# Kernel tuning notes

Hardware: AMD Instinct MI355X
Metric: run time of the kernel (lower is better)

## Reference

```python
import jax, jax.numpy as jnp
import numpy as np

SEQ = 8192
IN_DIM = 1024
HIDDEN_DIM = 2048
N_EXPERTS = 8
TOPK = 2


def setup_inputs() -> dict:
    key = jax.random.key(0)
    ks = jax.random.split(key, 6)
    scale = 0.02
    inp = jax.random.normal(ks[0], (SEQ, IN_DIM), jnp.float32)
    weights = jax.random.uniform(ks[1], (SEQ, TOPK), jnp.float32)
    selections = jax.random.randint(ks[2], (SEQ, TOPK), 0, N_EXPERTS, jnp.int32)
    up_proj = jax.random.normal(ks[3], (HIDDEN_DIM * N_EXPERTS, IN_DIM), jnp.float32) * scale
    gate_proj = jax.random.normal(ks[4], (HIDDEN_DIM * N_EXPERTS, IN_DIM), jnp.float32) * scale
    down_proj = jax.random.normal(ks[5], (HIDDEN_DIM * N_EXPERTS, IN_DIM), jnp.float32) * scale
    return {"inp": inp, "weights": weights, "up_proj": up_proj,
            "gate_proj": gate_proj, "down_proj": down_proj, "selections": selections}


def reference(inp, weights, up_proj, gate_proj, down_proj, selections):
    seq, in_dim = inp.shape
    topk = selections.shape[-1]
    # dispatch: replicate each token topk times -> (seq*topk, in_dim)
    x = jnp.broadcast_to(inp[:, None, :], (seq, topk, in_dim)).reshape(-1, in_dim)
    e_ids = selections.reshape(-1)  # (seq*topk,) expert id per dispatched token
    W_up = up_proj.reshape(N_EXPERTS, HIDDEN_DIM, in_dim)
    W_gate = gate_proj.reshape(N_EXPERTS, HIDDEN_DIM, in_dim)
    W_down = down_proj.reshape(N_EXPERTS, HIDDEN_DIM, in_dim)
    out = jnp.zeros_like(x)
    # grouped (block-sparse) GEMM: loop over the small fixed expert set,
    # masking tokens not routed to this expert (gelu(0)*0 = 0, so math matches).
    for e in range(N_EXPERTS):
        mask = (e_ids == e)[:, None]
        xe = jnp.where(mask, x, 0.0)
        h = xe @ W_up[e].T        # (seq*topk, hidden)
        g = xe @ W_gate[e].T      # (seq*topk, hidden)
        out = out + jnp.where(mask, (jax.nn.gelu(g) * h) @ W_down[e], 0.0)
    # combine: weighted sum over topk expert outputs per token
    return (out.reshape(seq, topk, in_dim) * weights[:, :, None]).sum(axis=1)
```

## Files before the change

kernel.cpp:

```cpp
#include <hip/hip_runtime.h>


#define SEQ 8192
#define IN_DIM 1024
#define HID 2048
#define NEXP 8
#define TOPK 2
#define NSLOT (SEQ * TOPK)

#define BM 128
#define BK 64
#define MAX_TILES 136

typedef unsigned short ushort_t;
typedef __bf16 bf16x8 __attribute__((ext_vector_type(8)));
typedef float f32x4 __attribute__((ext_vector_type(4)));

__device__ __forceinline__ ushort_t f2bf(float f) {
    union { float f; unsigned u; } v;
    v.f = f;
    unsigned r = v.u + 0x7FFFu + ((v.u >> 16) & 1u);
    return (ushort_t)(r >> 16);
}

__device__ __forceinline__ float gelu_tanh(float x) {
    float u = 0.7978845608028654f * x * (1.0f + 0.044715f * x * x);
    return x / (1.0f + __expf(-2.0f * u));
}

__device__ __forceinline__ void async16(const void* g, void* l) {
    __builtin_amdgcn_global_load_lds(
        (const __attribute__((address_space(1))) unsigned int*)g,
        (__attribute__((address_space(3))) unsigned int*)l, 16, 0, 0);
}

__device__ __forceinline__ void wait8_barrier() {
    asm volatile("s_waitcnt vmcnt(8)\ns_barrier" ::: "memory");
}
__device__ __forceinline__ void wait0_barrier() {
    asm volatile("s_waitcnt vmcnt(0)\ns_barrier" ::: "memory");
}
__device__ __forceinline__ void lds_barrier() {
    asm volatile("s_waitcnt lgkmcnt(0)\ns_barrier" ::: "memory");
}

__global__ void cast_bf16_kernel(const float* __restrict__ in,
                                 ushort_t* __restrict__ out, int n) {
    int i = (blockIdx.x * blockDim.x + threadIdx.x) * 4;
    if (i >= n) return;
    float4 v = *(const float4*)(in + i);
    union { ushort_t u[4]; uint2 v; } o;
    o.u[0] = f2bf(v.x); o.u[1] = f2bf(v.y);
    o.u[2] = f2bf(v.z); o.u[3] = f2bf(v.w);
    *(uint2*)(out + i) = o.v;
}

__global__ void transpose_cast_kernel(const float* __restrict__ in,
                                      ushort_t* __restrict__ out) {
    __shared__ float tile[32][33];
    int e = blockIdx.z;
    int d0 = blockIdx.x * 32, h0 = blockIdx.y * 32;
    int tx = threadIdx.x & 31, ty = threadIdx.x >> 5;
    const float* src = in + (size_t)e * HID * IN_DIM;
    for (int j = 0; j < 32; j += 8)
        tile[ty + j][tx] = src[(size_t)(h0 + ty + j) * IN_DIM + d0 + tx];
    __syncthreads();
    ushort_t* dst = out + (size_t)e * IN_DIM * HID;
    for (int j = 0; j < 32; j += 8)
        dst[(size_t)(d0 + ty + j) * HID + h0 + tx] = f2bf(tile[tx][ty + j]);
}

__global__ void route_kernel(const int* __restrict__ sel,
                             const float* __restrict__ wts,
                             int* __restrict__ meta,
                             int* __restrict__ stok,
                             int* __restrict__ sinv) {
    __shared__ int lc[256][NEXP];
    __shared__ int tot[NEXP];
    __shared__ int s_off[NEXP + 1];
    int t = threadIdx.x;
    int cnt[NEXP];
#pragma unroll
    for (int e = 0; e < NEXP; e++) cnt[e] = 0;
    int base = t * (NSLOT / 256);
    for (int i = 0; i < NSLOT / 256; i++) cnt[sel[base + i]]++;
#pragma unroll
    for (int e = 0; e < NEXP; e++) lc[t][e] = cnt[e];
    __syncthreads();
    if (t < NEXP) {
        int run = 0;
        for (int i = 0; i < 256; i++) { int v = lc[i][t]; lc[i][t] = run; run += v; }
        tot[t] = run;
    }
    __syncthreads();
    if (t == 0) {
        int o = 0;
        for (int e = 0; e < NEXP; e++) { s_off[e] = o; o += tot[e]; }
        s_off[NEXP] = o;
        for (int e = 0; e <= NEXP; e++) meta[e] = s_off[e];
        int nt = 0;
        for (int e = 0; e < NEXP; e++) {
            int c = s_off[e + 1] - s_off[e];
            int m = (c + BM - 1) / BM;
            for (int i = 0; i < m; i++) { meta[32 + 2 * nt] = e; meta[33 + 2 * nt] = i; nt++; }
        }
        meta[16] = nt;
    }
    __syncthreads();
    int cur[NEXP];
#pragma unroll
    for (int e = 0; e < NEXP; e++) cur[e] = s_off[e] + lc[t][e];
    for (int i = 0; i < NSLOT / 256; i++) {
        int slot = base + i;
        int e = sel[slot];
        int pos = cur[e]++;
        stok[pos] = slot >> 1;
        sinv[slot] = pos;
    }
}

__global__ __launch_bounds__(256) void gemm1_kernel(
    const ushort_t* __restrict__ X,
    const ushort_t* __restrict__ U,
    const ushort_t* __restrict__ G,
    const int* __restrict__ meta,
    const int* __restrict__ stok,
    ushort_t* __restrict__ act) {
    __shared__ __align__(16) ushort_t XT[2][BM * BK];
    __shared__ __align__(16) ushort_t UT[2][64 * BK];
    __shared__ __align__(16) ushort_t GT[2][64 * BK];
    __shared__ int s_tok[BM];

    int tile = blockIdx.x;
    if (tile >= meta[16]) return;
    int e = meta[32 + 2 * tile];
    int mt = meta[33 + 2 * tile];
    int off = meta[e];
    int cnt = meta[e + 1] - off;
    int m0 = mt * BM;
    int n0 = blockIdx.y * 64;

    int tid = threadIdx.x;
    if (tid < BM) {
        int r = m0 + tid;
        if (r >= cnt) r = cnt - 1;
        s_tok[tid] = stok[off + r];
    }
    __syncthreads();

    int lane = tid & 63;
    int w = tid >> 6;
    int wr = w >> 1, wc = w & 1;
    int srow = lane >> 3;
    int schunk = lane & 7;
    int gchunk = schunk ^ srow;

    const ushort_t* Ue = U + ((size_t)e * HID + n0) * IN_DIM;
    const ushort_t* Ge = G + ((size_t)e * HID + n0) * IN_DIM;

    const ushort_t* xp[4];
    const ushort_t* up2[2];
    const ushort_t* gp2[2];
#pragma unroll
    for (int i = 0; i < 4; i++) {
        int r = w * 32 + i * 8 + srow;
        xp[i] = X + (size_t)s_tok[r] * IN_DIM + gchunk * 8;
    }
#pragma unroll
    for (int i = 0; i < 2; i++) {
        int r = w * 16 + i * 8 + srow;
        up2[i] = Ue + (size_t)r * IN_DIM + gchunk * 8;
        gp2[i] = Ge + (size_t)r * IN_DIM + gchunk * 8;
    }

    f32x4 accH[4][2], accG[4][2];
#pragma unroll
    for (int mi = 0; mi < 4; mi++)
#pragma unroll
        for (int ni = 0; ni < 2; ni++) {
            accH[mi][ni] = (f32x4){0.f, 0.f, 0.f, 0.f};
            accG[mi][ni] = (f32x4){0.f, 0.f, 0.f, 0.f};
        }

    int r4 = lane & 15;
    int q = lane >> 4;
    int sw7 = r4 & 7;

#define G1_ISSUE(s)                                                        \
    {                                                                      \
        int _b = (s) & 1;                                                  \
        int _k0 = (s) * BK;                                                \
        _Pragma("unroll")                                                  \
        for (int i = 0; i < 4; i++)                                        \
            async16(xp[i] + _k0, &XT[_b][(w * 32 + i * 8) * BK]);          \
        _Pragma("unroll")                                                  \
        for (int i = 0; i < 2; i++) {                                      \
            async16(up2[i] + _k0, &UT[_b][(w * 16 + i * 8) * BK]);         \
            async16(gp2[i] + _k0, &GT[_b][(w * 16 + i * 8) * BK]);         \
        }                                                                  \
    }

#define G1_COMPUTE(s)                                                      \
    {                                                                      \
        int _b = (s) & 1;                                                  \
        _Pragma("unroll")                                                  \
        for (int kk = 0; kk < BK; kk += 32) {                              \
            int c = (kk >> 3) + q;                                         \
            int cs = ((c ^ sw7) << 3);                                     \
            bf16x8 a[4], bu[2], bg[2];                                     \
            _Pragma("unroll")                                              \
            for (int i = 0; i < 4; i++)                                    \
                a[i] = *(const bf16x8*)&XT[_b][(wr * 64 + i * 16 + r4) * BK + cs]; \
            _Pragma("unroll")                                              \
            for (int i = 0; i < 2; i++) {                                  \
                bu[i] = *(const bf16x8*)&UT[_b][(wc * 32 + i * 16 + r4) * BK + cs]; \
                bg[i] = *(const bf16x8*)&GT[_b][(wc * 32 + i * 16 + r4) * BK + cs]; \
            }                                                              \
            _Pragma("unroll")                                              \
            for (int mi = 0; mi < 4; mi++)                                 \
                _Pragma("unroll")                                          \
                for (int ni = 0; ni < 2; ni++) {                           \
                    accH[mi][ni] = __builtin_amdgcn_mfma_f32_16x16x32_bf16(\
                        a[mi], bu[ni], accH[mi][ni], 0, 0, 0);             \
                    accG[mi][ni] = __builtin_amdgcn_mfma_f32_16x16x32_bf16(\
                        a[mi], bg[ni], accG[mi][ni], 0, 0, 0);             \
                }                                                          \
        }                                                                  \
    }

    const int NK = IN_DIM / BK;
    G1_ISSUE(0);
    for (int s = 0; s < NK - 1; s++) {
        G1_ISSUE(s + 1);
        wait8_barrier();
        G1_COMPUTE(s);
        lds_barrier();
    }
    wait0_barrier();
    G1_COMPUTE(NK - 1);

#pragma unroll
    for (int mi = 0; mi < 4; mi++) {
#pragma unroll
        for (int r = 0; r < 4; r++) {
            int row_local = wr * 64 + mi * 16 + q * 4 + r;
            int grow = m0 + row_local;
            if (grow >= cnt) continue;
            size_t orow = (size_t)(off + grow) * HID + n0 + wc * 32;
#pragma unroll
            for (int ni = 0; ni < 2; ni++) {
                float h = accH[mi][ni][r];
                float g = accG[mi][ni][r];
                act[orow + ni * 16 + r4] = f2bf(gelu_tanh(g) * h);
            }
        }
    }
}

__global__ __launch_bounds__(256) void gemm2_kernel(
    const ushort_t* __restrict__ act,
    const ushort_t* __restrict__ DT,
    const int* __restrict__ meta,
    float* __restrict__ y) {
    __shared__ __align__(16) ushort_t AT[2][BM * BK];
    __shared__ __align__(16) ushort_t BT[2][BM * BK];

    int tile = blockIdx.x;
    if (tile >= meta[16]) return;
    int e = meta[32 + 2 * tile];
    int mt = meta[33 + 2 * tile];
    int off = meta[e];
    int cnt = meta[e + 1] - off;
    int m0 = mt * BM;
    int n0 = blockIdx.y * 128;

    int tid = threadIdx.x;
    int lane = tid & 63;
    int w = tid >> 6;
    int wr = w >> 1, wc = w & 1;
    int srow = lane >> 3;
    int schunk = lane & 7;
    int gchunk = schunk ^ srow;

    const ushort_t* Ae = act + (size_t)off * HID;
    const ushort_t* Be = DT + ((size_t)e * IN_DIM + n0) * HID;

    const ushort_t* ap[4];
    const ushort_t* bp[4];
#pragma unroll
    for (int i = 0; i < 4; i++) {
        int r = w * 32 + i * 8 + srow;
        int ar = m0 + r; if (ar >= cnt) ar = cnt - 1;
        ap[i] = Ae + (size_t)ar * HID + gchunk * 8;
        bp[i] = Be + (size_t)r * HID + gchunk * 8;
    }

    f32x4 acc[4][4];
#pragma unroll
    for (int mi = 0; mi < 4; mi++)
#pragma unroll
        for (int ni = 0; ni < 4; ni++) acc[mi][ni] = (f32x4){0.f, 0.f, 0.f, 0.f};

    int r4 = lane & 15;
    int q = lane >> 4;
    int sw7 = r4 & 7;

#define G2_ISSUE(s)                                                        \
    {                                                                      \
        int _b = (s) & 1;                                                  \
        int _k0 = (s) * BK;                                                \
        _Pragma("unroll")                                                  \
        for (int i = 0; i < 4; i++) {                                      \
            async16(ap[i] + _k0, &AT[_b][(w * 32 + i * 8) * BK]);          \
            async16(bp[i] + _k0, &BT[_b][(w * 32 + i * 8) * BK]);          \
        }                                                                  \
    }

#define G2_COMPUTE(s)                                                      \
    {                                                                      \
        int _b = (s) & 1;                                                  \
        _Pragma("unroll")                                                  \
        for (int kk = 0; kk < BK; kk += 32) {                              \
            int c = (kk >> 3) + q;                                         \
            int cs = ((c ^ sw7) << 3);                                     \
            bf16x8 a[4], b[4];                                             \
            _Pragma("unroll")                                              \
            for (int i = 0; i < 4; i++) {                                  \
                a[i] = *(const bf16x8*)&AT[_b][(wr * 64 + i * 16 + r4) * BK + cs]; \
                b[i] = *(const bf16x8*)&BT[_b][(wc * 64 + i * 16 + r4) * BK + cs]; \
            }                                                              \
            _Pragma("unroll")                                              \
            for (int mi = 0; mi < 4; mi++)                                 \
                _Pragma("unroll")                                          \
                for (int ni = 0; ni < 4; ni++)                             \
                    acc[mi][ni] = __builtin_amdgcn_mfma_f32_16x16x32_bf16( \
                        a[mi], b[ni], acc[mi][ni], 0, 0, 0);               \
        }                                                                  \
    }

    const int NK = HID / BK;
    G2_ISSUE(0);
    for (int s = 0; s < NK - 1; s++) {
        G2_ISSUE(s + 1);
        wait8_barrier();
        G2_COMPUTE(s);
        lds_barrier();
    }
    wait0_barrier();
    G2_COMPUTE(NK - 1);

#pragma unroll
    for (int mi = 0; mi < 4; mi++) {
#pragma unroll
        for (int r = 0; r < 4; r++) {
            int row_local = wr * 64 + mi * 16 + q * 4 + r;
            int grow = m0 + row_local;
            if (grow >= cnt) continue;
            float* orow = y + (size_t)(off + grow) * IN_DIM + n0 + wc * 64;
#pragma unroll
            for (int ni = 0; ni < 4; ni++)
                orow[ni * 16 + r4] = acc[mi][ni][r];
        }
    }
}

__global__ __launch_bounds__(256) void combine_kernel(
    const float* __restrict__ y,
    const float* __restrict__ wts,
    const int* __restrict__ sinv,
    float* __restrict__ out) {
    int tok = blockIdx.x;
    int c = threadIdx.x;
    int p0 = sinv[tok * 2], p1 = sinv[tok * 2 + 1];
    float w0 = wts[tok * 2], w1 = wts[tok * 2 + 1];
    float4 a = *(const float4*)(y + (size_t)p0 * IN_DIM + c * 4);
    float4 b = *(const float4*)(y + (size_t)p1 * IN_DIM + c * 4);
    float4 o;
    o.x = w0 * a.x + w1 * b.x;
    o.y = w0 * a.y + w1 * b.y;
    o.z = w0 * a.z + w1 * b.z;
    o.w = w0 * a.w + w1 * b.w;
    *(float4*)(out + (size_t)tok * IN_DIM + c * 4) = o;
}

extern "C" void kernel_launch(void* const* d_in, const int* in_sizes, int n_in,
                              void* d_out, int out_size, void* d_ws, size_t ws_size,
                              hipStream_t stream) {
    const float* inp  = (const float*)d_in[0];
    const float* wts  = (const float*)d_in[1];
    const float* up   = (const float*)d_in[2];
    const float* gate = (const float*)d_in[3];
    const float* down = (const float*)d_in[4];
    const int*   sel  = (const int*)d_in[5];
    float* out = (float*)d_out;

    char* ws = (char*)d_ws;
    ushort_t* inp_bf  = (ushort_t*)(ws);
    ushort_t* up_bf   = (ushort_t*)(ws + 16777216);
    ushort_t* gate_bf = (ushort_t*)(ws + 50331648);
    ushort_t* down_bf = (ushort_t*)(ws + 83886080);
    ushort_t* act     = (ushort_t*)(ws + 117440512);
    int*      stok    = (int*)(ws + 184549376);
    int*      sinv    = (int*)(ws + 184614912);
    int*      meta    = (int*)(ws + 184680448);
    float*    y       = (float*)(ws);

    cast_bf16_kernel<<<(SEQ * IN_DIM) / 1024, 256, 0, stream>>>(inp, inp_bf, SEQ * IN_DIM);
    cast_bf16_kernel<<<(NEXP * HID * IN_DIM) / 1024, 256, 0, stream>>>(up, up_bf, NEXP * HID * IN_DIM);
    cast_bf16_kernel<<<(NEXP * HID * IN_DIM) / 1024, 256, 0, stream>>>(gate, gate_bf, NEXP * HID * IN_DIM);
    transpose_cast_kernel<<<dim3(IN_DIM / 32, HID / 32, NEXP), 256, 0, stream>>>(down, down_bf);
    route_kernel<<<1, 256, 0, stream>>>(sel, wts, meta, stok, sinv);
    gemm1_kernel<<<dim3(MAX_TILES, HID / 64), 256, 0, stream>>>(inp_bf, up_bf, gate_bf, meta, stok, act);
    gemm2_kernel<<<dim3(MAX_TILES, IN_DIM / 128), 256, 0, stream>>>(act, down_bf, meta, y);
    combine_kernel<<<SEQ, 256, 0, stream>>>(y, wts, sinv, out);
}
```

Measured before the change: 610.5 us.

## Restructure gemm1 into 256x128 tiles with 8-wave ping-pong pipelined schedule

Gemm1 now uses 512-thread blocks computing 256x128 output tiles (up and gate) instead of 128x64, which roughly quarters the block count and raises data reuse per loaded tile. The K loop is rewritten as an explicit interleaved schedule: LDS reads, async global-to-LDS stores and MFMA clusters alternate, separated by barriers, waitcnt and s_setprio, so loads overlap compute. Tile-to-expert mapping is recomputed inline per block for the new tile size. The cost is a much larger accumulator register footprint and a schedule that depends on precise waitcnt counts, which carries some risk of spills or races.

```diff
diff --git a/kernel.cpp b/kernel.cpp
--- a/kernel.cpp
+++ b/kernel.cpp
@@ -11,6 +11,8 @@
 #define BM 128
 #define BK 64
 #define MAX_TILES 136
+#define BM1 256
+#define MAX_T1 72
 
 typedef unsigned short ushort_t;
 typedef __bf16 bf16x8 __attribute__((ext_vector_type(8)));
@@ -119,29 +121,35 @@
     }
 }
 
-__global__ __launch_bounds__(256) void gemm1_kernel(
+__global__ __launch_bounds__(512, 2) void gemm1_kernel(
     const ushort_t* __restrict__ X,
     const ushort_t* __restrict__ U,
     const ushort_t* __restrict__ G,
     const int* __restrict__ meta,
     const int* __restrict__ stok,
     ushort_t* __restrict__ act) {
-    __shared__ __align__(16) ushort_t XT[2][BM * BK];
-    __shared__ __align__(16) ushort_t UT[2][64 * BK];
-    __shared__ __align__(16) ushort_t GT[2][64 * BK];
-    __shared__ int s_tok[BM];
+    __shared__ __align__(16) ushort_t AT[2][2][128 * BK];
+    __shared__ __align__(16) ushort_t UT[2][128 * BK];
+    __shared__ __align__(16) ushort_t GT[2][128 * BK];
+    __shared__ int s_tok[BM1];
 
     int tile = blockIdx.x;
-    if (tile >= meta[16]) return;
-    int e = meta[32 + 2 * tile];
-    int mt = meta[33 + 2 * tile];
+    int e = -1, mt = 0, accT = 0;
+#pragma unroll
+    for (int ee = 0; ee < NEXP; ee++) {
+        int c = meta[ee + 1] - meta[ee];
+        int m = (c + BM1 - 1) >> 8;
+        if (tile >= accT && tile < accT + m) { e = ee; mt = tile - accT; }
+        accT += m;
+    }
+    if (e < 0) return;
     int off = meta[e];
     int cnt = meta[e + 1] - off;
-    int m0 = mt * BM;
-    int n0 = blockIdx.y * 64;
+    int m0 = mt * BM1;
+    int n0 = blockIdx.y * 128;
 
     int tid = threadIdx.x;
-    if (tid < BM) {
+    if (tid < BM1) {
         int r = m0 + tid;
         if (r >= cnt) r = cnt - 1;
         s_tok[tid] = stok[off + r];
@@ -150,111 +158,148 @@
 
     int lane = tid & 63;
     int w = tid >> 6;
-    int wr = w >> 1, wc = w & 1;
+    int wm = w >> 2;
+    int wn = w & 3;
     int srow = lane >> 3;
     int schunk = lane & 7;
     int gchunk = schunk ^ srow;
-
+    int r4 = lane & 15;
+    int q = lane >> 4;
+    int sw7 = r4 & 7;
+
+    const ushort_t* Xp[2][2];
+#pragma unroll
+    for (int h = 0; h < 2; h++)
+#pragma unroll
+        for (int j = 0; j < 2; j++) {
+            int r = h * 128 + w * 16 + j * 8 + srow;
+            Xp[h][j] = X + (size_t)s_tok[r] * IN_DIM + gchunk * 8;
+        }
     const ushort_t* Ue = U + ((size_t)e * HID + n0) * IN_DIM;
     const ushort_t* Ge = G + ((size_t)e * HID + n0) * IN_DIM;
-
-    const ushort_t* xp[4];
-    const ushort_t* up2[2];
-    const ushort_t* gp2[2];
-#pragma unroll
-    for (int i = 0; i < 4; i++) {
-        int r = w * 32 + i * 8 + srow;
-        xp[i] = X + (size_t)s_tok[r] * IN_DIM + gchunk * 8;
-    }
-#pragma unroll
-    for (int i = 0; i < 2; i++) {
-        int r = w * 16 + i * 8 + srow;
-        up2[i] = Ue + (size_t)r * IN_DIM + gchunk * 8;
-        gp2[i] = Ge + (size_t)r * IN_DIM + gchunk * 8;
-    }
-
-    f32x4 accH[4][2], accG[4][2];
-#pragma unroll
-    for (int mi = 0; mi < 4; mi++)
+    const ushort_t* Upt[2];
+    const ushort_t* Gpt[2];
+#pragma unroll
+    for (int j = 0; j < 2; j++) {
+        int r = w * 16 + j * 8 + srow;
+        Upt[j] = Ue + (size_t)r * IN_DIM + gchunk * 8;
+        Gpt[j] = Ge + (size_t)r * IN_DIM + gchunk * 8;
+    }
+
+    f32x4 accH[8][2], accG[8][2];
+#pragma unroll
+    for (int mi = 0; mi < 8; mi++)
 #pragma unroll
         for (int ni = 0; ni < 2; ni++) {
             accH[mi][ni] = (f32x4){0.f, 0.f, 0.f, 0.f};
             accG[mi][ni] = (f32x4){0.f, 0.f, 0.f, 0.f};
         }
 
-    int r4 = lane & 15;
-    int q = lane >> 4;
-    int sw7 = r4 & 7;
-
-#define G1_ISSUE(s)                                                        \
-    {                                                                      \
-        int _b = (s) & 1;                                                  \
-        int _k0 = (s) * BK;                                                \
-        _Pragma("unroll")                                                  \
-        for (int i = 0; i < 4; i++)                                        \
-            async16(xp[i] + _k0, &XT[_b][(w * 32 + i * 8) * BK]);          \
-        _Pragma("unroll")                                                  \
-        for (int i = 0; i < 2; i++) {                                      \
-            async16(up2[i] + _k0, &UT[_b][(w * 16 + i * 8) * BK]);         \
-            async16(gp2[i] + _k0, &GT[_b][(w * 16 + i * 8) * BK]);         \
-        }                                                                  \
-    }
-
-#define G1_COMPUTE(s)                                                      \
-    {                                                                      \
-        int _b = (s) & 1;                                                  \
-        _Pragma("unroll")                                                  \
-        for (int kk = 0; kk < BK; kk += 32) {                              \
-            int c = (kk >> 3) + q;                                         \
-            int cs = ((c ^ sw7) << 3);                                     \
-            bf16x8 a[4], bu[2], bg[2];                                     \
-            _Pragma("unroll")                                              \
-            for (int i = 0; i < 4; i++)                                    \
-                a[i] = *(const bf16x8*)&XT[_b][(wr * 64 + i * 16 + r4) * BK + cs]; \
-            _Pragma("unroll")                                              \
-            for (int i = 0; i < 2; i++) {                                  \
-                bu[i] = *(const bf16x8*)&UT[_b][(wc * 32 + i * 16 + r4) * BK + cs]; \
-                bg[i] = *(const bf16x8*)&GT[_b][(wc * 32 + i * 16 + r4) * BK + cs]; \
-            }                                                              \
-            _Pragma("unroll")                                              \
-            for (int mi = 0; mi < 4; mi++)                                 \
-                _Pragma("unroll")                                          \
-                for (int ni = 0; ni < 2; ni++) {                           \
-                    accH[mi][ni] = __builtin_amdgcn_mfma_f32_16x16x32_bf16(\
-                        a[mi], bu[ni], accH[mi][ni], 0, 0, 0);             \
-                    accG[mi][ni] = __builtin_amdgcn_mfma_f32_16x16x32_bf16(\
-                        a[mi], bg[ni], accG[mi][ni], 0, 0, 0);             \
-                }                                                          \
-        }                                                                  \
-    }
-
-    const int NK = IN_DIM / BK;
-    G1_ISSUE(0);
-    for (int s = 0; s < NK - 1; s++) {
-        G1_ISSUE(s + 1);
-        wait8_barrier();
-        G1_COMPUTE(s);
-        lds_barrier();
-    }
-    wait0_barrier();
-    G1_COMPUTE(NK - 1);
-
-#pragma unroll
-    for (int mi = 0; mi < 4; mi++) {
+    bf16x8 a[4][2], bu[2][2], bg[2][2];
+
+#define ST_A(b, h, kt) {                                                   \
+        async16(Xp[h][0] + (kt), &AT[b][h][(w * 16) * BK]);                \
+        async16(Xp[h][1] + (kt), &AT[b][h][(w * 16 + 8) * BK]); }
+#define ST_U(b, kt) {                                                      \
+        async16(Upt[0] + (kt), &UT[b][(w * 16) * BK]);                     \
+        async16(Upt[1] + (kt), &UT[b][(w * 16 + 8) * BK]); }
+#define ST_G(b, kt) {                                                      \
+        async16(Gpt[0] + (kt), &GT[b][(w * 16) * BK]);                     \
+        async16(Gpt[1] + (kt), &GT[b][(w * 16 + 8) * BK]); }
+
+#define RD_A(b, mb) {                                                      \
+        _Pragma("unroll") for (int mi = 0; mi < 4; mi++)                   \
+        _Pragma("unroll") for (int kh = 0; kh < 2; kh++)                   \
+            a[mi][kh] = *(const bf16x8*)&AT[b][wm][                        \
+                ((mb) + mi * 16 + r4) * BK + (((kh * 4 + q) ^ sw7) << 3)]; }
+#define RD_U(b) {                                                          \
+        _Pragma("unroll") for (int ni = 0; ni < 2; ni++)                   \
+        _Pragma("unroll") for (int kh = 0; kh < 2; kh++)                   \
+            bu[ni][kh] = *(const bf16x8*)&UT[b][                           \
+                (wn * 32 + ni * 16 + r4) * BK + (((kh * 4 + q) ^ sw7) << 3)]; }
+#define RD_G(b) {                                                          \
+        _Pragma("unroll") for (int ni = 0; ni < 2; ni++)                   \
+        _Pragma("unroll") for (int kh = 0; kh < 2; kh++)                   \
+            bg[ni][kh] = *(const bf16x8*)&GT[b][                           \
+                (wn * 32 + ni * 16 + r4) * BK + (((kh * 4 + q) ^ sw7) << 3)]; }
+
+#define MM(ACC, mb2, BB) {                                                 \
+        _Pragma("unroll") for (int mi = 0; mi < 4; mi++)                   \
+        _Pragma("unroll") for (int ni = 0; ni < 2; ni++)                   \
+        _Pragma("unroll") for (int kh = 0; kh < 2; kh++)                   \
+            ACC[(mb2) + mi][ni] = __builtin_amdgcn_mfma_f32_16x16x32_bf16( \
+                a[mi][kh], BB[ni][kh], ACC[(mb2) + mi][ni], 0, 0, 0); }
+
+#define BARRIER __builtin_amdgcn_s_barrier()
+#define LGKM0 asm volatile("s_waitcnt lgkmcnt(0)" ::: "memory")
+#define VMW2 asm volatile("s_waitcnt vmcnt(2)" ::: "memory")
+#define PRIO1 __builtin_amdgcn_s_setprio(1)
+#define PRIO0 __builtin_amdgcn_s_setprio(0)
+
+    ST_A(0, 0, 0); ST_A(0, 1, 0); ST_U(0, 0); ST_G(0, 0);
+    ST_A(1, 0, BK);
+    VMW2; BARRIER;
+
+    for (int it = 0; it < 8; it++) {
+        int t = 2 * it;
+        int k1 = (t + 1) * BK;
+        int k2 = (t + 2 < 16 ? t + 2 : 15) * BK;
+        int k3 = (t + 3 < 16 ? t + 3 : 15) * BK;
+        RD_A(0, 0); RD_U(0);
+        ST_A(1, 1, k1);
+        BARRIER; LGKM0;
+        PRIO1; MM(accH, 0, bu); PRIO0; BARRIER;
+        RD_G(0);
+        ST_U(1, k1);
+        BARRIER; LGKM0;
+        PRIO1; MM(accG, 0, bg); PRIO0; BARRIER;
+        RD_A(0, 64);
+        ST_G(1, k1);
+        BARRIER; LGKM0;
+        PRIO1; MM(accG, 4, bg); PRIO0; BARRIER;
+        ST_A(0, 0, k2);
+        VMW2; BARRIER;
+        PRIO1; MM(accH, 4, bu); PRIO0; BARRIER;
+        RD_A(1, 0); RD_U(1);
+        ST_A(0, 1, k2);
+        BARRIER; LGKM0;
+        PRIO1; MM(accH, 0, bu); PRIO0; BARRIER;
+        RD_G(1);
+        ST_U(0, k2);
+        BARRIER; LGKM0;
+        PRIO1; MM(accG, 0, bg); PRIO0; BARRIER;
+        RD_A(1, 64);
+        ST_G(0, k2);
+        BARRIER; LGKM0;
+        PRIO1; MM(accG, 4, bg); PRIO0; BARRIER;
+        ST_A(1, 0, k3);
+        VMW2; BARRIER;
+        PRIO1; MM(accH, 4, bu); PRIO0; BARRIER;
+    }
+
+#pragma unroll
+    for (int mf = 0; mf < 8; mf++) {
 #pragma unroll
         for (int r = 0; r < 4; r++) {
-            int row_local = wr * 64 + mi * 16 + q * 4 + r;
+            int row_local = wm * 128 + mf * 16 + q * 4 + r;
             int grow = m0 + row_local;
             if (grow >= cnt) continue;
-            size_t orow = (size_t)(off + grow) * HID + n0 + wc * 32;
+            size_t orow = (size_t)(off + grow) * HID + n0 + wn * 32;
 #pragma unroll
             for (int ni = 0; ni < 2; ni++) {
-                float h = accH[mi][ni][r];
-                float g = accG[mi][ni][r];
+                float h = accH[mf][ni][r];
+                float g = accG[mf][ni][r];
                 act[orow + ni * 16 + r4] = f2bf(gelu_tanh(g) * h);
             }
         }
     }
+#undef ST_A
+#undef ST_U
+#undef ST_G
+#undef RD_A
+#undef RD_U
+#undef RD_G
+#undef MM
 }
 
 __global__ __launch_bounds__(256) void gemm2_kernel(
@@ -410,7 +455,7 @@
     cast_bf16_kernel<<<(NEXP * HID * IN_DIM) / 1024, 256, 0, stream>>>(gate, gate_bf, NEXP * HID * IN_DIM);
     transpose_cast_kernel<<<dim3(IN_DIM / 32, HID / 32, NEXP), 256, 0, stream>>>(down, down_bf);
     route_kernel<<<1, 256, 0, stream>>>(sel, wts, meta, stok, sinv);
-    gemm1_kernel<<<dim3(MAX_TILES, HID / 64), 256, 0, stream>>>(inp_bf, up_bf, gate_bf, meta, stok, act);
+    gemm1_kernel<<<dim3(MAX_T1, HID / 128), 512, 0, stream>>>(inp_bf, up_bf, gate_bf, meta, stok, act);
     gemm2_kernel<<<dim3(MAX_TILES, IN_DIM / 128), 256, 0, stream>>>(act, down_bf, meta, y);
     combine_kernel<<<SEQ, 256, 0, stream>>>(y, wts, sinv, out);
 }
```

Result: faster. 573.2 us (-6.1%).
